# Optimization experiments

Hardware: AMD Instinct MI355X
Metric: run time of the kernel (lower is better)

Reference implementation:

```python
import jax, jax.numpy as jnp
import numpy as np

HEADS = 4
DIM_HEAD = 32
SCALE = 16.0
EPS = 1e-5  # jax.nn.standardize default


def _standardize(t):
    # standardize over last axis (the flattened x*y*z sequence), per (b, h, d)
    mu = jnp.mean(t, axis=-1, keepdims=True)
    var = jnp.var(t, axis=-1, keepdims=True)
    return (t - mu) * jax.lax.rsqrt(var + EPS)


def setup_inputs() -> dict:
    key = jax.random.key(0)
    k1, k2, k3 = jax.random.split(key, 3)
    dim = 64
    hidden = HEADS * DIM_HEAD  # 128
    b, x, y, z = 2, 16, 16, 16
    inp = jax.random.normal(k1, (b, x, y, z, dim), dtype=jnp.float32)
    # 1x1x1 convs == pointwise channel matmuls; init like flax lecun_normal-ish scale
    w_qkv = jax.random.normal(k2, (dim, 3 * hidden), dtype=jnp.float32) / np.sqrt(dim)
    w_out = jax.random.normal(k3, (hidden, dim), dtype=jnp.float32) / np.sqrt(hidden)
    b_out = jnp.zeros((dim,), dtype=jnp.float32)
    return {"input": inp, "w_qkv": w_qkv, "w_out": w_out, "b_out": b_out}


def reference(input, w_qkv, w_out, b_out):
    b, x, y, z, c = input.shape
    s = x * y * z
    # pointwise conv -> qkv
    qkv = jnp.einsum('bxyzc,cd->bxyzd', input, w_qkv)  # [b,x,y,z,3*hidden]
    q, k, v = jnp.split(qkv, 3, axis=-1)
    # rearrange 'b x y z (h c) -> b h c (x y z)'
    def to_bhds(t):
        return t.reshape(b, s, HEADS, DIM_HEAD).transpose(0, 2, 3, 1)  # [b,h,d,s]
    q, k, v = map(to_bhds, (q, k, v))
    q = _standardize(q)
    k = _standardize(k)
    sim = jnp.einsum('bhdi,bhdj->bhij', q, k) * SCALE  # [b,h,s,s]
    attn = jax.nn.softmax(sim, axis=-1)
    out = jnp.einsum('bhij,bhdj->bhid', attn, v)  # [b,h,s,d]
    # rearrange 'b h (x y z) d -> b x y z (h d)'
    out = out.transpose(0, 2, 1, 3).reshape(b, x, y, z, HEADS * DIM_HEAD)
    return jnp.einsum('bxyzc,co->bxyzo', out, w_out) + b_out
```

## Files before the change

### kernel.cpp

```cpp
#include <hip/hip_runtime.h>
#include <math.h>
#include <stdint.h>


typedef __attribute__((ext_vector_type(8))) short short8;
typedef __attribute__((ext_vector_type(4))) float f32x4;

#define QSCALE 23.083120654223414f

#if __has_builtin(__builtin_amdgcn_exp2f)
#define EXP2F(x) __builtin_amdgcn_exp2f(x)
#else
#define EXP2F(x) exp2f(x)
#endif

__device__ inline uint32_t pack_hilo(float y) {
  uint32_t uy = __float_as_uint(y);
  uint32_t hb = (uy + 0x7fffu + ((uy >> 16) & 1u)) >> 16;
  float hf = __uint_as_float(hb << 16);
  float r = y - hf;
  uint32_t ur = __float_as_uint(r);
  uint32_t lb = (ur + 0x7fffu + ((ur >> 16) & 1u)) >> 16;
  return (hb << 16) | (lb & 0xffffu);
}

__device__ inline ushort f32_to_bf16(float y) {
  uint32_t uy = __float_as_uint(y);
  return (ushort)((uy + 0x7fffu + ((uy >> 16) & 1u)) >> 16);
}

__device__ inline float bpermf(int addr, float v) {
  return __int_as_float(__builtin_amdgcn_ds_bpermute(addr, __float_as_int(v)));
}

__global__ __launch_bounds__(256) void qkv_kernel(const float* __restrict__ in,
                                                  const float* __restrict__ w,
                                                  float* __restrict__ qf,
                                                  float* __restrict__ kf,
                                                  ushort* __restrict__ vhg,
                                                  float* __restrict__ psum,
                                                  float* __restrict__ psq) {
  __shared__ float As[64][68];
  __shared__ float Bs[64][68];
  __shared__ float ssum[64], ssq[64];
  const int ctile = blockIdx.x % 6;
  const int stile = blockIdx.x / 6;
  const int tid = threadIdx.x;
  const int row0 = stile * 64;
  const int sel = ctile >> 1;

  if (tid < 64) { ssum[tid] = 0.f; ssq[tid] = 0.f; }
  for (int idx = tid; idx < 64 * 64; idx += 256) {
    int s = idx >> 6, c = idx & 63;
    As[s][c] = in[(size_t)(row0 + s) * 64 + c];
  }
  for (int idx = tid; idx < 64 * 64; idx += 256) {
    int c = idx >> 6, ch = idx & 63;
    Bs[c][ch] = w[(size_t)c * 384 + ctile * 64 + ch];
  }
  __syncthreads();

  const int ts = tid >> 4, tc = tid & 15;
  float acc[4][4] = {};
  for (int c = 0; c < 64; c += 4) {
    float4 av[4];
#pragma unroll
    for (int a = 0; a < 4; ++a) av[a] = *(const float4*)&As[ts * 4 + a][c];
    const float4 b0 = *(const float4*)&Bs[c + 0][tc * 4];
    const float4 b1 = *(const float4*)&Bs[c + 1][tc * 4];
    const float4 b2 = *(const float4*)&Bs[c + 2][tc * 4];
    const float4 b3 = *(const float4*)&Bs[c + 3][tc * 4];
    const float bm[4][4] = {{b0.x, b0.y, b0.z, b0.w},
                            {b1.x, b1.y, b1.z, b1.w},
                            {b2.x, b2.y, b2.z, b2.w},
                            {b3.x, b3.y, b3.z, b3.w}};
#pragma unroll
    for (int a = 0; a < 4; ++a) {
      const float aw[4] = {av[a].x, av[a].y, av[a].z, av[a].w};
#pragma unroll
      for (int j = 0; j < 4; ++j)
#pragma unroll
        for (int cc = 0; cc < 4; ++cc) acc[a][cc] = fmaf(aw[j], bm[j][cc], acc[a][cc]);
    }
  }

  const int b = row0 >> 12;
  const int sl = (row0 & 4095) + ts * 4;
  const int chg0 = ctile * 64 + tc * 4;

  if (sel < 2) {
    const int hd0 = chg0 & 127;
    const int h = hd0 >> 5, d0 = hd0 & 31;
    float* dst = (sel == 0 ? qf : kf) + ((size_t)(b * 4 + h) * 4096) * 32 + d0;
#pragma unroll
    for (int a = 0; a < 4; ++a) {
      float4 st = make_float4(acc[a][0], acc[a][1], acc[a][2], acc[a][3]);
      *(float4*)&dst[(size_t)(sl + a) * 32] = st;
    }
#pragma unroll
    for (int cc = 0; cc < 4; ++cc) {
      float sm = acc[0][cc] + acc[1][cc] + acc[2][cc] + acc[3][cc];
      float sq = acc[0][cc] * acc[0][cc] + acc[1][cc] * acc[1][cc] +
                 acc[2][cc] * acc[2][cc] + acc[3][cc] * acc[3][cc];
      atomicAdd(&ssum[tc * 4 + cc], sm);
      atomicAdd(&ssq[tc * 4 + cc], sq);
    }
    __syncthreads();
    if (tid < 64) {
      const int ch = (ctile & 1) * 64 + tid;
      const int idx = (((sel * 2 + b) * 128) + ch) * 64 + (stile & 63);
      psum[idx] = ssum[tid];
      psq[idx] = ssq[tid];
    }
  } else {
#pragma unroll
    for (int cc = 0; cc < 4; ++cc) {
      const int hd = (chg0 + cc) & 127;
      const int h = hd >> 5, d = hd & 31;
      ushort4 st;
      st.x = f32_to_bf16(acc[0][cc]);
      st.y = f32_to_bf16(acc[1][cc]);
      st.z = f32_to_bf16(acc[2][cc]);
      st.w = f32_to_bf16(acc[3][cc]);
      *(ushort4*)&vhg[((size_t)(b * 4 + h) * 32 + d) * 4096 + sl] = st;
    }
  }
}

__global__ __launch_bounds__(256) void norm_kernel(const float* __restrict__ kf,
                                                   ushort* __restrict__ khg,
                                                   ushort* __restrict__ klg,
                                                   const float* __restrict__ psum,
                                                   const float* __restrict__ psq,
                                                   float* __restrict__ qA,
                                                   float* __restrict__ qB) {
  const int bx = blockIdx.x;
  const int tid = threadIdx.x;
  if (bx == 128) {
    const int base = (((tid >> 7) * 128) + (tid & 127)) * 64;
    float sm = 0.f, sq = 0.f;
#pragma unroll 8
    for (int e = 0; e < 64; ++e) {
      sm += psum[base + e];
      sq += psq[base + e];
    }
    const float mu = sm * (1.f / 4096.f);
    const float inv = rsqrtf(sq * (1.f / 4096.f) - mu * mu + 1e-5f) * QSCALE;
    qA[tid] = inv;
    qB[tid] = -mu * inv;
    return;
  }
  __shared__ float red[2][32][8];
  __shared__ float kA[32], kB[32];
  const int bh = bx >> 4;
  const int s0 = (bx & 15) * 256;
  {
    const int d = tid >> 3, p = tid & 7;
    const int base = ((2 + (bh >> 2)) * 128 + (bh & 3) * 32 + d) * 64 + p * 8;
    float sm = 0.f, sq = 0.f;
#pragma unroll
    for (int e = 0; e < 8; ++e) {
      sm += psum[base + e];
      sq += psq[base + e];
    }
    red[0][d][p] = sm;
    red[1][d][p] = sq;
  }
  __syncthreads();
  if (tid < 32) {
    float sm = 0.f, sq = 0.f;
#pragma unroll
    for (int e = 0; e < 8; ++e) {
      sm += red[0][tid][e];
      sq += red[1][tid][e];
    }
    const float mu = sm * (1.f / 4096.f);
    const float inv = rsqrtf(sq * (1.f / 4096.f) - mu * mu + 1e-5f);
    kA[tid] = inv;
    kB[tid] = -mu * inv;
  }
  __syncthreads();

  const int d0 = (tid & 7) * 4;
  const float A0 = kA[d0], A1 = kA[d0 + 1], A2 = kA[d0 + 2], A3 = kA[d0 + 3];
  const float B0 = kB[d0], B1 = kB[d0 + 1], B2 = kB[d0 + 2], B3 = kB[d0 + 3];
  const float* src = kf + ((size_t)bh * 4096 + s0) * 32;
  ushort* dh = khg + ((size_t)bh * 4096 + s0) * 32 + d0;
  ushort* dl = klg + ((size_t)bh * 4096 + s0) * 32 + d0;
#pragma unroll
  for (int i = 0; i < 8; ++i) {
    const int s = (tid + i * 256) >> 3;
    float4 x = *(const float4*)&src[(size_t)s * 32 + d0];
    float y[4] = {fmaf(x.x, A0, B0), fmaf(x.y, A1, B1), fmaf(x.z, A2, B2), fmaf(x.w, A3, B3)};
    ushort4 hi, lo;
    ushort* hp = (ushort*)&hi;
    ushort* lp = (ushort*)&lo;
#pragma unroll
    for (int e = 0; e < 4; ++e) {
      uint32_t pk = pack_hilo(y[e]);
      hp[e] = (ushort)(pk >> 16);
      lp[e] = (ushort)(pk & 0xffff);
    }
    *(ushort4*)&dh[(size_t)s * 32] = hi;
    *(ushort4*)&dl[(size_t)s * 32] = lo;
  }
}

__global__ __launch_bounds__(1024, 8) void attn_kernel(const float* __restrict__ qf,
                                                       const float* __restrict__ qA,
                                                       const float* __restrict__ qB,
                                                       const ushort* __restrict__ khg,
                                                       const ushort* __restrict__ klg,
                                                       const ushort* __restrict__ vhg,
                                                       float* __restrict__ o) {
  __shared__ char lds[49152];

  const int tid = threadIdx.x;
  const int strm = tid >> 8;
  const int st = tid & 255;
  const int w = st >> 6;
  const int lane = tid & 63;
  const int q = lane >> 4, tl = lane & 15;
  const int bh = blockIdx.x >> 6;
  const int i0 = (blockIdx.x & 63) * 64;

  ushort* KHI = (ushort*)lds + strm * 6144;
  ushort* KLO = KHI + 2048;
  ushort* VHI = KHI + 4096;

  const int irow = i0 + w * 16 + tl;
  const float* qptr = qf + ((size_t)bh * 4096 + irow) * 32 + q * 8;
  short8 qhi, qlo;
  {
    const float4 xa = *(const float4*)qptr;
    const float4 xb = *(const float4*)(qptr + 4);
    const float4 Aa = *(const float4*)&qA[bh * 32 + q * 8];
    const float4 Ab = *(const float4*)&qA[bh * 32 + q * 8 + 4];
    const float4 Ba = *(const float4*)&qB[bh * 32 + q * 8];
    const float4 Bb = *(const float4*)&qB[bh * 32 + q * 8 + 4];
    const float y[8] = {fmaf(xa.x, Aa.x, Ba.x), fmaf(xa.y, Aa.y, Ba.y),
                        fmaf(xa.z, Aa.z, Ba.z), fmaf(xa.w, Aa.w, Ba.w),
                        fmaf(xb.x, Ab.x, Bb.x), fmaf(xb.y, Ab.y, Bb.y),
                        fmaf(xb.z, Ab.z, Bb.z), fmaf(xb.w, Ab.w, Bb.w)};
#pragma unroll
    for (int j = 0; j < 8; ++j) {
      uint32_t pk = pack_hilo(y[j]);
      qhi[j] = (short)(pk >> 16);
      qlo[j] = (short)(pk & 0xffff);
    }
  }

  const int bp16 = (lane ^ 16) << 2;
  const int bp32 = (lane ^ 32) << 2;

  const int jr = st >> 2, ck = st & 3;
  const int sig = ((((jr >> 5) & 1) * 2 + ((jr >> 2) & 1)) << 4) +
                  ((((jr >> 3) & 3)) << 2) + (jr & 3);
  const int ckp = ck ^ ((sig >> 1) & 3);
  const ushort* khsrc = khg + ((size_t)bh * 4096 + jr) * 32 + ck * 8;
  const ushort* klsrc = klg + ((size_t)bh * 4096 + jr) * 32 + ck * 8;
  ushort* khdst = &KHI[sig * 32 + ckp * 8];
  ushort* kldst = &KLO[sig * 32 + ckp * 8];
  const int dr = st >> 3, cv = st & 7;
  const int cvp = cv ^ (dr & 7);
  const ushort* vsrc = vhg + ((size_t)bh * 32 + dr) * 4096 + cv * 8;
  ushort* vdst = &VHI[dr * 64 + cvp * 8];

  const int koff = tl * 32 + (q ^ ((tl >> 1) & 3)) * 8;
  const int voff0 = tl * 64 + (q ^ (tl & 7)) * 8;
  const int voff1 = tl * 64 + ((q + 4) ^ (tl & 7)) * 8;

  f32x4 oacc[2] = {{0.f, 0.f, 0.f, 0.f}, {0.f, 0.f, 0.f, 0.f}};
  float m = -INFINITY, l = 0.f;

  uint4 rk = *(const uint4*)(khsrc + (size_t)(strm * 1024) * 32);
  uint4 rl = *(const uint4*)(klsrc + (size_t)(strm * 1024) * 32);
  uint4 rv = *(const uint4*)(vsrc + strm * 1024);

  for (int it = 0; it < 16; ++it) {
    __syncthreads();
    *(uint4*)khdst = rk;
    *(uint4*)kldst = rl;
    *(uint4*)vdst = rv;
    __syncthreads();
    if (it < 15) {
      const int j0n = strm * 1024 + (it + 1) * 64;
      rk = *(const uint4*)(khsrc + (size_t)j0n * 32);
      rl = *(const uint4*)(klsrc + (size_t)j0n * 32);
      rv = *(const uint4*)(vsrc + j0n);
    }

    f32x4 sc[4];
#pragma unroll
    for (int jt = 0; jt < 4; ++jt) {
      short8 kh = *(const short8*)&KHI[jt * 512 + koff];
      short8 kl = *(const short8*)&KLO[jt * 512 + koff];
      f32x4 z = {0.f, 0.f, 0.f, 0.f};
      z = __builtin_amdgcn_mfma_f32_16x16x32_bf16(kh, qhi, z, 0, 0, 0);
      z = __builtin_amdgcn_mfma_f32_16x16x32_bf16(kh, qlo, z, 0, 0, 0);
      z = __builtin_amdgcn_mfma_f32_16x16x32_bf16(kl, qhi, z, 0, 0, 0);
      sc[jt] = z;
    }

    f32x4 vm = __builtin_elementwise_max(__builtin_elementwise_max(sc[0], sc[1]),
                                         __builtin_elementwise_max(sc[2], sc[3]));
    float mx = fmaxf(fmaxf(vm[0], vm[1]), fmaxf(vm[2], vm[3]));
    mx = fmaxf(mx, bpermf(bp16, mx));
    mx = fmaxf(mx, bpermf(bp32, mx));
    const float mn = fmaxf(m, mx);
    const float al = EXP2F(m - mn);
    m = mn;
#pragma unroll
    for (int jt = 0; jt < 4; ++jt) {
      f32x4 t = sc[jt] - mn;
#pragma unroll
      for (int r = 0; r < 4; ++r) sc[jt][r] = EXP2F(t[r]);
    }
    f32x4 vs = (sc[0] + sc[1]) + (sc[2] + sc[3]);
    float rs = (vs[0] + vs[1]) + (vs[2] + vs[3]);
    rs += bpermf(bp16, rs);
    rs += bpermf(bp32, rs);
    l = l * al + rs;
    oacc[0] *= al;
    oacc[1] *= al;

    uint32_t pk[8];
#pragma unroll
    for (int jt = 0; jt < 4; ++jt)
#pragma unroll
      for (int p = 0; p < 2; ++p)
        pk[jt * 2 + p] = __builtin_amdgcn_perm(__float_as_uint(sc[jt][2 * p + 1]),
                                               __float_as_uint(sc[jt][2 * p]), 0x07060302u);
    union { uint32_t u[4]; short8 s; } c0, c1;
    c0.u[0] = pk[0]; c0.u[1] = pk[1]; c0.u[2] = pk[2]; c0.u[3] = pk[3];
    c1.u[0] = pk[4]; c1.u[1] = pk[5]; c1.u[2] = pk[6]; c1.u[3] = pk[7];

#pragma unroll
    for (int dt = 0; dt < 2; ++dt) {
      short8 va0 = *(const short8*)&VHI[dt * 1024 + voff0];
      short8 va1 = *(const short8*)&VHI[dt * 1024 + voff1];
      f32x4 z = oacc[dt];
      z = __builtin_amdgcn_mfma_f32_16x16x32_bf16(va0, c0.s, z, 0, 0, 0);
      z = __builtin_amdgcn_mfma_f32_16x16x32_bf16(va1, c1.s, z, 0, 0, 0);
      oacc[dt] = z;
    }
  }

  __syncthreads();
  float* OM = (float*)lds;
  float* ML = (float*)(lds + 36864);
  {
    float* om = OM + ((size_t)(strm * 64 + w * 16 + tl)) * 36;
    *(f32x4*)&om[q * 4] = oacc[0];
    *(f32x4*)&om[16 + q * 4] = oacc[1];
    if (q == 0) {
      ML[strm * 128 + w * 16 + tl] = m;
      ML[strm * 128 + 64 + w * 16 + tl] = l;
    }
  }
  __syncthreads();
  const int b = bh >> 2, h = bh & 3;
#pragma unroll
  for (int pass = 0; pass < 2; ++pass) {
    const int idx = tid + pass * 1024;
    const int i = idx >> 5, d = idx & 31;
    const float m0 = ML[i], m1 = ML[128 + i], m2 = ML[256 + i], m3 = ML[384 + i];
    const float l0 = ML[64 + i], l1 = ML[192 + i], l2 = ML[320 + i], l3 = ML[448 + i];
    const float M = fmaxf(fmaxf(m0, m1), fmaxf(m2, m3));
    const float w0 = EXP2F(m0 - M), w1 = EXP2F(m1 - M);
    const float w2 = EXP2F(m2 - M), w3 = EXP2F(m3 - M);
    const float L = l0 * w0 + l1 * w1 + l2 * w2 + l3 * w3;
    const float val = (OM[i * 36 + d] * w0 + OM[(64 + i) * 36 + d] * w1 +
                       OM[(128 + i) * 36 + d] * w2 + OM[(192 + i) * 36 + d] * w3) *
                      (1.001953125f / L);
    o[((size_t)(b * 4096) + i0 + i) * 128 + h * 32 + d] = val;
  }
}

__global__ __launch_bounds__(256) void proj_kernel(const float* __restrict__ o,
                                                   const float* __restrict__ w,
                                                   const float* __restrict__ bias,
                                                   float* __restrict__ out) {
  __shared__ float wT[64 * 132];
  const int tid = threadIdx.x;
  for (int idx = tid; idx < 8192; idx += 256) {
    const int c = idx >> 6, col = idx & 63;
    const int g = (c >> 2) ^ ((col >> 3) & 7);
    wT[col * 132 + (g << 2) + (c & 3)] = w[idx];
  }
  __syncthreads();
  const int col = tid & 63;
  const int r = blockIdx.x * 8 + ((tid >> 6) << 1);
  const float* r0 = o + (size_t)r * 128;
  const float* r1 = r0 + 128;
  const int wbase = col * 132;
  const int gx = (col >> 3) & 7;
  float a0 = bias[col], a1 = a0;
  for (int c = 0; c < 128; c += 4) {
    const float4 x0 = *(const float4*)&r0[c];
    const float4 x1 = *(const float4*)&r1[c];
    const float4 wv = *(const float4*)&wT[wbase + ((((c >> 2) ^ gx)) << 2)];
    a0 = fmaf(x0.x, wv.x, a0); a0 = fmaf(x0.y, wv.y, a0);
    a0 = fmaf(x0.z, wv.z, a0); a0 = fmaf(x0.w, wv.w, a0);
    a1 = fmaf(x1.x, wv.x, a1); a1 = fmaf(x1.y, wv.y, a1);
    a1 = fmaf(x1.z, wv.z, a1); a1 = fmaf(x1.w, wv.w, a1);
  }
  out[(size_t)r * 64 + col] = a0;
  out[(size_t)(r + 1) * 64 + col] = a1;
}

extern "C" void kernel_launch(void* const* d_in, const int* in_sizes, int n_in,
                              void* d_out, int out_size, void* d_ws, size_t ws_size,
                              hipStream_t stream) {
  const float* input = (const float*)d_in[0];
  const float* w_qkv = (const float*)d_in[1];
  const float* w_out = (const float*)d_in[2];
  const float* b_out = (const float*)d_in[3];

  char* W = (char*)d_ws;
  float* qf = (float*)(W + 0);
  float* kf = (float*)(W + (4u << 20));
  ushort* khg = (ushort*)(W + (8u << 20));
  ushort* klg = (ushort*)(W + (10u << 20));
  ushort* vhg = (ushort*)(W + (12u << 20));
  float* psum = (float*)(W + (14u << 20));
  float* psq = (float*)(W + (14u << 20) + (128u << 10));
  float* qA = (float*)(W + (14u << 20) + (256u << 10));
  float* qB = qA + 256;
  float* ob = kf;
  float* out = (float*)d_out;

  hipLaunchKernelGGL(qkv_kernel, dim3(768), dim3(256), 0, stream, input, w_qkv, qf, kf,
                     vhg, psum, psq);
  hipLaunchKernelGGL(norm_kernel, dim3(129), dim3(256), 0, stream, kf, khg, klg,
                     psum, psq, qA, qB);
  hipLaunchKernelGGL(attn_kernel, dim3(512), dim3(1024), 0, stream, qf, qA, qB,
                     khg, klg, vhg, ob);
  hipLaunchKernelGGL(proj_kernel, dim3(1024), dim3(256), 0, stream, ob, w_out, b_out, out);
}
```

Measured before the change: 144.7 us.

## Switch attention to 32x32x16 MFMA with 512-thread blocks and coalesced V stores

The attention kernel moves from 16x16x32 bf16 MFMA tiles to 32x32x16 tiles, so each wave covers 32 query rows. Blocks shrink from 1024 to 512 threads, and each thread loads twice as much K/V per iteration; the register prefetch of the next tile is dropped. The QKV kernel now stages V through LDS so it can write coalesced 16-byte bf16 rows instead of scattered 8-byte stores. Larger MFMAs mean fewer instructions and fewer cross-lane reductions, at the cost of more accumulator registers and losing the load/compute overlap.

```diff
diff --git a/kernel.cpp b/kernel.cpp
--- a/kernel.cpp
+++ b/kernel.cpp
@@ -5,6 +5,7 @@
 
 typedef __attribute__((ext_vector_type(8))) short short8;
 typedef __attribute__((ext_vector_type(4))) float f32x4;
+typedef __attribute__((ext_vector_type(16))) float f32x16;
 
 #define QSCALE 23.083120654223414f
 
@@ -113,16 +114,27 @@
       psq[idx] = ssq[tid];
     }
   } else {
-#pragma unroll
-    for (int cc = 0; cc < 4; ++cc) {
-      const int hd = (chg0 + cc) & 127;
+    __syncthreads();
+    float* VT = &As[0][0];
+#pragma unroll
+    for (int cc = 0; cc < 4; ++cc)
+      *(float4*)&VT[(tc * 4 + cc) * 68 + ts * 4] =
+          make_float4(acc[0][cc], acc[1][cc], acc[2][cc], acc[3][cc]);
+    __syncthreads();
+#pragma unroll
+    for (int t2 = 0; t2 < 2; ++t2) {
+      const int lin = tid + t2 * 256;
+      const int ch = lin >> 3, gg = lin & 7;
+      const float4 f0 = *(const float4*)&VT[ch * 68 + gg * 8];
+      const float4 f1 = *(const float4*)&VT[ch * 68 + gg * 8 + 4];
+      uint4 pk;
+      pk.x = (uint32_t)f32_to_bf16(f0.x) | ((uint32_t)f32_to_bf16(f0.y) << 16);
+      pk.y = (uint32_t)f32_to_bf16(f0.z) | ((uint32_t)f32_to_bf16(f0.w) << 16);
+      pk.z = (uint32_t)f32_to_bf16(f1.x) | ((uint32_t)f32_to_bf16(f1.y) << 16);
+      pk.w = (uint32_t)f32_to_bf16(f1.z) | ((uint32_t)f32_to_bf16(f1.w) << 16);
+      const int hd = (ctile * 64 + ch) & 127;
       const int h = hd >> 5, d = hd & 31;
-      ushort4 st;
-      st.x = f32_to_bf16(acc[0][cc]);
-      st.y = f32_to_bf16(acc[1][cc]);
-      st.z = f32_to_bf16(acc[2][cc]);
-      st.w = f32_to_bf16(acc[3][cc]);
-      *(ushort4*)&vhg[((size_t)(b * 4 + h) * 32 + d) * 4096 + sl] = st;
+      *(uint4*)&vhg[((size_t)(b * 4 + h) * 32 + d) * 4096 + (row0 & 4095) + gg * 8] = pk;
     }
   }
 }
@@ -206,143 +218,153 @@
   }
 }
 
-__global__ __launch_bounds__(1024, 8) void attn_kernel(const float* __restrict__ qf,
-                                                       const float* __restrict__ qA,
-                                                       const float* __restrict__ qB,
-                                                       const ushort* __restrict__ khg,
-                                                       const ushort* __restrict__ klg,
-                                                       const ushort* __restrict__ vhg,
-                                                       float* __restrict__ o) {
+__global__ __launch_bounds__(512, 4) void attn_kernel(const float* __restrict__ qf,
+                                                      const float* __restrict__ qA,
+                                                      const float* __restrict__ qB,
+                                                      const ushort* __restrict__ khg,
+                                                      const ushort* __restrict__ klg,
+                                                      const ushort* __restrict__ vhg,
+                                                      float* __restrict__ o) {
   __shared__ char lds[49152];
 
   const int tid = threadIdx.x;
-  const int strm = tid >> 8;
-  const int st = tid & 255;
-  const int w = st >> 6;
+  const int strm = tid >> 7;
+  const int st = tid & 127;
+  const int wv = (tid >> 6) & 1;
   const int lane = tid & 63;
-  const int q = lane >> 4, tl = lane & 15;
+  const int pl = lane & 31;
+  const int h2 = lane >> 5;
   const int bh = blockIdx.x >> 6;
   const int i0 = (blockIdx.x & 63) * 64;
 
   ushort* KHI = (ushort*)lds + strm * 6144;
-  ushort* KLO = KHI + 2048;
-  ushort* VHI = KHI + 4096;
-
-  const int irow = i0 + w * 16 + tl;
-  const float* qptr = qf + ((size_t)bh * 4096 + irow) * 32 + q * 8;
-  short8 qhi, qlo;
+
+  const int irow = i0 + wv * 32 + pl;
+  const float* qptr = qf + ((size_t)bh * 4096 + irow) * 32;
+  short8 qh0, ql0, qh1, ql1;
   {
-    const float4 xa = *(const float4*)qptr;
-    const float4 xb = *(const float4*)(qptr + 4);
-    const float4 Aa = *(const float4*)&qA[bh * 32 + q * 8];
-    const float4 Ab = *(const float4*)&qA[bh * 32 + q * 8 + 4];
-    const float4 Ba = *(const float4*)&qB[bh * 32 + q * 8];
-    const float4 Bb = *(const float4*)&qB[bh * 32 + q * 8 + 4];
-    const float y[8] = {fmaf(xa.x, Aa.x, Ba.x), fmaf(xa.y, Aa.y, Ba.y),
-                        fmaf(xa.z, Aa.z, Ba.z), fmaf(xa.w, Aa.w, Ba.w),
-                        fmaf(xb.x, Ab.x, Bb.x), fmaf(xb.y, Ab.y, Bb.y),
-                        fmaf(xb.z, Ab.z, Bb.z), fmaf(xb.w, Ab.w, Bb.w)};
+    const int da = 8 * h2, db = 16 + 8 * h2;
+    const float4 x0 = *(const float4*)(qptr + da);
+    const float4 x1 = *(const float4*)(qptr + da + 4);
+    const float4 x2 = *(const float4*)(qptr + db);
+    const float4 x3 = *(const float4*)(qptr + db + 4);
+    const float4 A0 = *(const float4*)&qA[bh * 32 + da];
+    const float4 A1 = *(const float4*)&qA[bh * 32 + da + 4];
+    const float4 A2 = *(const float4*)&qA[bh * 32 + db];
+    const float4 A3 = *(const float4*)&qA[bh * 32 + db + 4];
+    const float4 B0 = *(const float4*)&qB[bh * 32 + da];
+    const float4 B1 = *(const float4*)&qB[bh * 32 + da + 4];
+    const float4 B2 = *(const float4*)&qB[bh * 32 + db];
+    const float4 B3 = *(const float4*)&qB[bh * 32 + db + 4];
+    const float y0[8] = {fmaf(x0.x, A0.x, B0.x), fmaf(x0.y, A0.y, B0.y),
+                         fmaf(x0.z, A0.z, B0.z), fmaf(x0.w, A0.w, B0.w),
+                         fmaf(x1.x, A1.x, B1.x), fmaf(x1.y, A1.y, B1.y),
+                         fmaf(x1.z, A1.z, B1.z), fmaf(x1.w, A1.w, B1.w)};
+    const float y1[8] = {fmaf(x2.x, A2.x, B2.x), fmaf(x2.y, A2.y, B2.y),
+                         fmaf(x2.z, A2.z, B2.z), fmaf(x2.w, A2.w, B2.w),
+                         fmaf(x3.x, A3.x, B3.x), fmaf(x3.y, A3.y, B3.y),
+                         fmaf(x3.z, A3.z, B3.z), fmaf(x3.w, A3.w, B3.w)};
 #pragma unroll
     for (int j = 0; j < 8; ++j) {
-      uint32_t pk = pack_hilo(y[j]);
-      qhi[j] = (short)(pk >> 16);
-      qlo[j] = (short)(pk & 0xffff);
-    }
-  }
-
-  const int bp16 = (lane ^ 16) << 2;
+      uint32_t p0 = pack_hilo(y0[j]);
+      uint32_t p1 = pack_hilo(y1[j]);
+      qh0[j] = (short)(p0 >> 16); ql0[j] = (short)(p0 & 0xffff);
+      qh1[j] = (short)(p1 >> 16); ql1[j] = (short)(p1 & 0xffff);
+    }
+  }
+
   const int bp32 = (lane ^ 32) << 2;
 
   const int jr = st >> 2, ck = st & 3;
-  const int sig = ((((jr >> 5) & 1) * 2 + ((jr >> 2) & 1)) << 4) +
-                  ((((jr >> 3) & 3)) << 2) + (jr & 3);
-  const int ckp = ck ^ ((sig >> 1) & 3);
-  const ushort* khsrc = khg + ((size_t)bh * 4096 + jr) * 32 + ck * 8;
-  const ushort* klsrc = klg + ((size_t)bh * 4096 + jr) * 32 + ck * 8;
-  ushort* khdst = &KHI[sig * 32 + ckp * 8];
-  ushort* kldst = &KLO[sig * 32 + ckp * 8];
+  const int et = jr >> 4, eh = (jr >> 3) & 1, ee = jr & 7;
+  const int pphys = (ee & 3) + 8 * (ee >> 2) + 4 * eh + 16 * (et & 1);
+  const int rowp = (et >> 1) * 32 + pphys;
+  const int ckp = ck ^ ((pphys >> 1) & 2);
+  const ushort* ksrc = khg + ((size_t)bh * 4096 + jr) * 32 + ck * 8;
+  const ushort* lsrc = klg + ((size_t)bh * 4096 + jr) * 32 + ck * 8;
+  ushort* kdst = KHI + rowp * 32 + ckp * 8;
   const int dr = st >> 3, cv = st & 7;
-  const int cvp = cv ^ (dr & 7);
   const ushort* vsrc = vhg + ((size_t)bh * 32 + dr) * 4096 + cv * 8;
-  ushort* vdst = &VHI[dr * 64 + cvp * 8];
-
-  const int koff = tl * 32 + (q ^ ((tl >> 1) & 3)) * 8;
-  const int voff0 = tl * 64 + (q ^ (tl & 7)) * 8;
-  const int voff1 = tl * 64 + ((q + 4) ^ (tl & 7)) * 8;
-
-  f32x4 oacc[2] = {{0.f, 0.f, 0.f, 0.f}, {0.f, 0.f, 0.f, 0.f}};
+  ushort* vdst = KHI + 4096 + dr * 64 + (cv ^ (dr & 7)) * 8;
+
+  const int sw = (pl >> 1) & 2;
+  const int k00 = pl * 32 + (h2 ^ sw) * 8;
+  const int k01 = pl * 32 + ((2 + h2) ^ sw) * 8;
+  int voff[4];
+#pragma unroll
+  for (int t = 0; t < 4; ++t) voff[t] = pl * 64 + ((2 * t + h2) ^ (pl & 7)) * 8;
+
+  f32x16 oacc;
+#pragma unroll
+  for (int r = 0; r < 16; ++r) oacc[r] = 0.f;
   float m = -INFINITY, l = 0.f;
 
-  uint4 rk = *(const uint4*)(khsrc + (size_t)(strm * 1024) * 32);
-  uint4 rl = *(const uint4*)(klsrc + (size_t)(strm * 1024) * 32);
-  uint4 rv = *(const uint4*)(vsrc + strm * 1024);
-
   for (int it = 0; it < 16; ++it) {
+    const int j0 = strm * 1024 + it * 64;
     __syncthreads();
-    *(uint4*)khdst = rk;
-    *(uint4*)kldst = rl;
-    *(uint4*)vdst = rv;
+    {
+      const uint4 ka0 = *(const uint4*)(ksrc + (size_t)j0 * 32);
+      const uint4 ka1 = *(const uint4*)(ksrc + (size_t)j0 * 32 + 1024);
+      const uint4 la0 = *(const uint4*)(lsrc + (size_t)j0 * 32);
+      const uint4 la1 = *(const uint4*)(lsrc + (size_t)j0 * 32 + 1024);
+      const uint4 va0 = *(const uint4*)(vsrc + j0);
+      const uint4 va1 = *(const uint4*)(vsrc + j0 + 65536);
+      *(uint4*)kdst = ka0;
+      *(uint4*)(kdst + 1024) = ka1;
+      *(uint4*)(kdst + 2048) = la0;
+      *(uint4*)(kdst + 3072) = la1;
+      *(uint4*)vdst = va0;
+      *(uint4*)(vdst + 1024) = va1;
+    }
     __syncthreads();
-    if (it < 15) {
-      const int j0n = strm * 1024 + (it + 1) * 64;
-      rk = *(const uint4*)(khsrc + (size_t)j0n * 32);
-      rl = *(const uint4*)(klsrc + (size_t)j0n * 32);
-      rv = *(const uint4*)(vsrc + j0n);
-    }
-
-    f32x4 sc[4];
-#pragma unroll
-    for (int jt = 0; jt < 4; ++jt) {
-      short8 kh = *(const short8*)&KHI[jt * 512 + koff];
-      short8 kl = *(const short8*)&KLO[jt * 512 + koff];
-      f32x4 z = {0.f, 0.f, 0.f, 0.f};
-      z = __builtin_amdgcn_mfma_f32_16x16x32_bf16(kh, qhi, z, 0, 0, 0);
-      z = __builtin_amdgcn_mfma_f32_16x16x32_bf16(kh, qlo, z, 0, 0, 0);
-      z = __builtin_amdgcn_mfma_f32_16x16x32_bf16(kl, qhi, z, 0, 0, 0);
-      sc[jt] = z;
-    }
-
-    f32x4 vm = __builtin_elementwise_max(__builtin_elementwise_max(sc[0], sc[1]),
-                                         __builtin_elementwise_max(sc[2], sc[3]));
-    float mx = fmaxf(fmaxf(vm[0], vm[1]), fmaxf(vm[2], vm[3]));
-    mx = fmaxf(mx, bpermf(bp16, mx));
-    mx = fmaxf(mx, bpermf(bp32, mx));
-    const float mn = fmaxf(m, mx);
-    const float al = EXP2F(m - mn);
-    m = mn;
-#pragma unroll
-    for (int jt = 0; jt < 4; ++jt) {
-      f32x4 t = sc[jt] - mn;
-#pragma unroll
-      for (int r = 0; r < 4; ++r) sc[jt][r] = EXP2F(t[r]);
-    }
-    f32x4 vs = (sc[0] + sc[1]) + (sc[2] + sc[3]);
-    float rs = (vs[0] + vs[1]) + (vs[2] + vs[3]);
-    rs += bpermf(bp16, rs);
-    rs += bpermf(bp32, rs);
-    l = l * al + rs;
-    oacc[0] *= al;
-    oacc[1] *= al;
-
-    uint32_t pk[8];
-#pragma unroll
-    for (int jt = 0; jt < 4; ++jt)
-#pragma unroll
-      for (int p = 0; p < 2; ++p)
-        pk[jt * 2 + p] = __builtin_amdgcn_perm(__float_as_uint(sc[jt][2 * p + 1]),
-                                               __float_as_uint(sc[jt][2 * p]), 0x07060302u);
-    union { uint32_t u[4]; short8 s; } c0, c1;
-    c0.u[0] = pk[0]; c0.u[1] = pk[1]; c0.u[2] = pk[2]; c0.u[3] = pk[3];
-    c1.u[0] = pk[4]; c1.u[1] = pk[5]; c1.u[2] = pk[6]; c1.u[3] = pk[7];
-
-#pragma unroll
-    for (int dt = 0; dt < 2; ++dt) {
-      short8 va0 = *(const short8*)&VHI[dt * 1024 + voff0];
-      short8 va1 = *(const short8*)&VHI[dt * 1024 + voff1];
-      f32x4 z = oacc[dt];
-      z = __builtin_amdgcn_mfma_f32_16x16x32_bf16(va0, c0.s, z, 0, 0, 0);
-      z = __builtin_amdgcn_mfma_f32_16x16x32_bf16(va1, c1.s, z, 0, 0, 0);
-      oacc[dt] = z;
+
+#pragma unroll
+    for (int u = 0; u < 2; ++u) {
+      const ushort* KB = KHI + u * 1024;
+      const short8 kh0 = *(const short8*)(KB + k00);
+      const short8 kh1 = *(const short8*)(KB + k01);
+      const short8 kl0 = *(const short8*)(KB + 2048 + k00);
+      const short8 kl1 = *(const short8*)(KB + 2048 + k01);
+      f32x16 sc;
+#pragma unroll
+      for (int r = 0; r < 16; ++r) sc[r] = 0.f;
+      sc = __builtin_amdgcn_mfma_f32_32x32x16_bf16(kh0, qh0, sc, 0, 0, 0);
+      sc = __builtin_amdgcn_mfma_f32_32x32x16_bf16(kh1, qh1, sc, 0, 0, 0);
+      sc = __builtin_amdgcn_mfma_f32_32x32x16_bf16(kh0, ql0, sc, 0, 0, 0);
+      sc = __builtin_amdgcn_mfma_f32_32x32x16_bf16(kh1, ql1, sc, 0, 0, 0);
+      sc = __builtin_amdgcn_mfma_f32_32x32x16_bf16(kl0, qh0, sc, 0, 0, 0);
+      sc = __builtin_amdgcn_mfma_f32_32x32x16_bf16(kl1, qh1, sc, 0, 0, 0);
+
+      float mx = sc[0];
+#pragma unroll
+      for (int r = 1; r < 16; ++r) mx = fmaxf(mx, sc[r]);
+      mx = fmaxf(mx, bpermf(bp32, mx));
+      const float mn = fmaxf(m, mx);
+      const float al = EXP2F(m - mn);
+      m = mn;
+#pragma unroll
+      for (int r = 0; r < 16; ++r) sc[r] = EXP2F(sc[r] - mn);
+      float rs = 0.f;
+#pragma unroll
+      for (int r = 0; r < 16; ++r) rs += sc[r];
+      rs += bpermf(bp32, rs);
+      l = l * al + rs;
+#pragma unroll
+      for (int r = 0; r < 16; ++r) oacc[r] *= al;
+
+      uint32_t pk[8];
+#pragma unroll
+      for (int i = 0; i < 8; ++i)
+        pk[i] = __builtin_amdgcn_perm(__float_as_uint(sc[2 * i + 1]),
+                                      __float_as_uint(sc[2 * i]), 0x07060302u);
+      union { uint32_t u4[4]; short8 s8; } p0, p1;
+      p0.u4[0] = pk[0]; p0.u4[1] = pk[1]; p0.u4[2] = pk[2]; p0.u4[3] = pk[3];
+      p1.u4[0] = pk[4]; p1.u4[1] = pk[5]; p1.u4[2] = pk[6]; p1.u4[3] = pk[7];
+
+      const short8 va0 = *(const short8*)(KHI + 4096 + voff[2 * u]);
+      const short8 va1 = *(const short8*)(KHI + 4096 + voff[2 * u + 1]);
+      oacc = __builtin_amdgcn_mfma_f32_32x32x16_bf16(va0, p0.s8, oacc, 0, 0, 0);
+      oacc = __builtin_amdgcn_mfma_f32_32x32x16_bf16(va1, p1.s8, oacc, 0, 0, 0);
     }
   }
 
@@ -350,19 +372,21 @@
   float* OM = (float*)lds;
   float* ML = (float*)(lds + 36864);
   {
-    float* om = OM + ((size_t)(strm * 64 + w * 16 + tl)) * 36;
-    *(f32x4*)&om[q * 4] = oacc[0];
-    *(f32x4*)&om[16 + q * 4] = oacc[1];
-    if (q == 0) {
-      ML[strm * 128 + w * 16 + tl] = m;
-      ML[strm * 128 + 64 + w * 16 + tl] = l;
+    float* om = OM + (size_t)(strm * 64 + wv * 32 + pl) * 36;
+#pragma unroll
+    for (int g = 0; g < 4; ++g)
+      *(float4*)&om[4 * h2 + 8 * g] =
+          make_float4(oacc[4 * g], oacc[4 * g + 1], oacc[4 * g + 2], oacc[4 * g + 3]);
+    if (h2 == 0) {
+      ML[strm * 128 + wv * 32 + pl] = m;
+      ML[strm * 128 + 64 + wv * 32 + pl] = l;
     }
   }
   __syncthreads();
   const int b = bh >> 2, h = bh & 3;
 #pragma unroll
-  for (int pass = 0; pass < 2; ++pass) {
-    const int idx = tid + pass * 1024;
+  for (int pass = 0; pass < 4; ++pass) {
+    const int idx = tid + pass * 512;
     const int i = idx >> 5, d = idx & 31;
     const float m0 = ML[i], m1 = ML[128 + i], m2 = ML[256 + i], m3 = ML[384 + i];
     const float l0 = ML[64 + i], l1 = ML[192 + i], l2 = ML[320 + i], l3 = ML[448 + i];
@@ -434,7 +458,7 @@
                      vhg, psum, psq);
   hipLaunchKernelGGL(norm_kernel, dim3(129), dim3(256), 0, stream, kf, khg, klg,
                      psum, psq, qA, qB);
-  hipLaunchKernelGGL(attn_kernel, dim3(512), dim3(1024), 0, stream, qf, qA, qB,
+  hipLaunchKernelGGL(attn_kernel, dim3(512), dim3(512), 0, stream, qf, qA, qB,
                      khg, klg, vhg, ob);
   hipLaunchKernelGGL(proj_kernel, dim3(1024), dim3(256), 0, stream, ob, w_out, b_out, out);
 }
```

Measured after the change: 147.6 us. Within noise of the previous version (+2.0%).
